# Kernel tuning notes

Hardware: AMD Instinct MI355X
Metric: run time of the kernel (lower is better)

Reference implementation:

```python
import jax, jax.numpy as jnp
import numpy as np

B, N, D, H, F = 2, 2048, 512, 8, 8
HD = D // H

def setup_inputs() -> dict:
    key = jax.random.key(0)
    ks = jax.random.split(key, 11)
    s = 1.0 / np.sqrt(D)
    return {
        "x": jax.random.normal(ks[0], (B, N, D), dtype=jnp.float32),
        "phase_coords": jax.random.uniform(ks[1], (B, N, F), dtype=jnp.float32) * 6.28,
        "Wq": jax.random.normal(ks[2], (D, D), dtype=jnp.float32) * s,
        "bq": jax.random.normal(ks[3], (D,), dtype=jnp.float32) * 0.01,
        "Wk": jax.random.normal(ks[4], (D, D), dtype=jnp.float32) * s,
        "bk": jax.random.normal(ks[5], (D,), dtype=jnp.float32) * 0.01,
        "Wv": jax.random.normal(ks[6], (D, D), dtype=jnp.float32) * s,
        "bv": jax.random.normal(ks[7], (D,), dtype=jnp.float32) * 0.01,
        "Wo": jax.random.normal(ks[8], (D, D), dtype=jnp.float32) * s,
        "bo": jax.random.normal(ks[9], (D,), dtype=jnp.float32) * 0.01,
        "phase_bias": jax.random.normal(ks[10], (H, F), dtype=jnp.float32) * 0.1,
    }

def reference(x, phase_coords, Wq, bq, Wk, bk, Wv, bv, Wo, bo, phase_bias):
    b, n, _ = x.shape
    def proj(W, bias):
        # [B,N,D] -> [B,H,N,HD]
        return (x @ W.T + bias).reshape(b, n, H, HD).transpose(0, 2, 1, 3)
    Q, K, V = proj(Wq, bq), proj(Wk, bk), proj(Wv, bv)
    scores = jnp.einsum("bhqd,bhkd->bhqk", Q, K) / np.sqrt(HD)
    # phase coherence bias: cos of pairwise phase diffs, weighted per head
    phase_diff = phase_coords[:, :, None, :] - phase_coords[:, None, :, :]  # [B,N,N,F]
    coherence = jnp.cos(phase_diff)
    bias = jnp.einsum("bqkf,hf->bhqk", coherence, phase_bias)
    scores = scores + bias
    attn = jax.nn.softmax(scores, axis=-1)
    attended = jnp.einsum("bhqk,bhkd->bhqd", attn, V)
    attended = attended.transpose(0, 2, 1, 3).reshape(b, n, D)
    return attended @ Wo.T + bo
```

## Files before the change

### kernel.cpp

```cpp
#include <hip/hip_runtime.h>
#include <stdint.h>

typedef unsigned short u16;
typedef unsigned int   u32;
typedef __bf16 bf16x8 __attribute__((ext_vector_type(8)));
typedef float  f32x4  __attribute__((ext_vector_type(4)));
typedef u16    u16x8  __attribute__((ext_vector_type(8)));
typedef u16    u16x4  __attribute__((ext_vector_type(4)));

#define B_  2
#define N_  2048
#define D_  512
#define H_  8
#define HD_ 64
#define LOG2E 1.4426950408889634f

__device__ __forceinline__ u16 f2bf(float f) {
  union { float f; u32 u; } v; v.f = f;
  u32 r = v.u + 0x7FFFu + ((v.u >> 16) & 1u);
  return (u16)(r >> 16);
}
__device__ __forceinline__ u16 f2bf_trunc(float f) {
  union { float f; u32 u; } v; v.f = f;
  return (u16)(v.u >> 16);
}
__device__ __forceinline__ float bf2f(u16 s) {
  union { u32 u; float f; } v; v.u = ((u32)s) << 16; return v.f;
}
__device__ __forceinline__ void gload_lds16(const void* g, void* l) {
  __builtin_amdgcn_global_load_lds(
      (const __attribute__((address_space(1))) void*)g,
      (__attribute__((address_space(3))) void*)l, 16, 0, 0);
}
__device__ __forceinline__ void gload_lds4(const void* g, void* l) {
  __builtin_amdgcn_global_load_lds(
      (const __attribute__((address_space(1))) void*)g,
      (__attribute__((address_space(3))) void*)l, 4, 0, 0);
}

__global__ __launch_bounds__(256) void k_prep(
    const float* __restrict__ x, const float* __restrict__ pc,
    const float* __restrict__ Wq, const float* __restrict__ bq,
    const float* __restrict__ Wk, const float* __restrict__ bk,
    const float* __restrict__ Wv, const float* __restrict__ bv,
    const float* __restrict__ Wo,
    u16* __restrict__ xb, u16* __restrict__ wqkvb, float* __restrict__ bqkv,
    u16* __restrict__ wob, u16* __restrict__ pcs)
{
  int gid = blockIdx.x * blockDim.x + threadIdx.x;
  int stride = gridDim.x * blockDim.x;
  const float qs = 0.125f * LOG2E;
  for (int i = gid; i < B_ * N_ * D_; i += stride) xb[i] = f2bf(x[i]);
  for (int i = gid; i < 3 * D_ * D_; i += stride) {
    int r = i >> 9;
    float v;
    if (r < 512)       v = Wq[i] * qs;
    else if (r < 1024) v = Wk[i - 512 * 512];
    else               v = Wv[i - 1024 * 512];
    wqkvb[i] = f2bf(v);
  }
  for (int i = gid; i < 3 * D_; i += stride) {
    float v;
    if (i < 512)       v = bq[i] * qs;
    else if (i < 1024) v = bk[i - 512];
    else               v = bv[i - 1024];
    bqkv[i] = v;
  }
  for (int i = gid; i < D_ * D_; i += stride) wob[i] = f2bf(Wo[i]);
  for (int i = gid; i < B_ * N_; i += stride) {
#pragma unroll
    for (int f = 0; f < 8; f++) {
      float a = pc[i * 8 + f];
      pcs[i * 16 + f]     = f2bf(__cosf(a));
      pcs[i * 16 + 8 + f] = f2bf(__sinf(a));
    }
  }
}

template <int MODE, int BN>
__global__ __launch_bounds__(256) void k_gemm(
    const u16* __restrict__ A, const u16* __restrict__ Bm,
    const float* __restrict__ bias,
    u16* __restrict__ Qp, u16* __restrict__ Kp, u16* __restrict__ Vt,
    float* __restrict__ Of)
{
  constexpr int JT  = BN / 32;
  constexpr int BNC = BN / 32;
  __shared__ u16 As[3][64 * 64];
  __shared__ u16 Bs[3][BN * 64];
  const int tid = threadIdx.x;
  const int wave = tid >> 6, lane = tid & 63;
  const int fr = lane & 15, kg = lane >> 4;
  const int m0 = blockIdx.x * 64, n0 = blockIdx.y * BN;
  const int wr = (wave >> 1) * 32, wc = (wave & 1) * (BN / 2);

  f32x4 acc[2][JT];
#pragma unroll
  for (int i = 0; i < 2; i++)
#pragma unroll
    for (int j = 0; j < JT; j++)
#pragma unroll
      for (int r = 0; r < 4; r++) acc[i][j][r] = 0.f;

  auto stage = [&](int buf, int k0) {
#pragma unroll
    for (int u = 0; u < 2; u++) {
      int chunk = (wave * 2 + u) * 64 + lane;
      int row = chunk >> 3, cl = chunk & 7;
      gload_lds16(A + (size_t)(m0 + row) * 512 + k0 + ((cl ^ (row & 7)) << 3),
                  &As[buf][(wave * 2 + u) * 512]);
    }
#pragma unroll
    for (int u = 0; u < BNC; u++) {
      int chunk = (wave * BNC + u) * 64 + lane;
      int row = chunk >> 3, cl = chunk & 7;
      gload_lds16(Bm + (size_t)(n0 + row) * 512 + k0 + ((cl ^ (row & 7)) << 3),
                  &Bs[buf][(wave * BNC + u) * 512]);
    }
  };

  stage(0, 0);
  stage(1, 64);

#pragma unroll
  for (int s = 0; s < 8; s++) {
    if (s < 7) {
      if constexpr (BN == 128) asm volatile("s_waitcnt vmcnt(6)" ::: "memory");
      else                     asm volatile("s_waitcnt vmcnt(4)" ::: "memory");
    } else {
      asm volatile("s_waitcnt vmcnt(0)" ::: "memory");
    }
    asm volatile("s_waitcnt lgkmcnt(0)" ::: "memory");
    __builtin_amdgcn_sched_barrier(0);
    __builtin_amdgcn_s_barrier();
    __builtin_amdgcn_sched_barrier(0);
    if (s < 6) stage((s + 2) % 3, (s + 2) * 64);
    const int cb = s % 3;
#pragma unroll
    for (int ksub = 0; ksub < 2; ksub++) {
      bf16x8 af[2], bf[JT];
#pragma unroll
      for (int i = 0; i < 2; i++)
        af[i] = *(const bf16x8*)&As[cb][(wr + i * 16 + fr) * 64 + (((ksub * 4 + kg) ^ (fr & 7)) << 3)];
#pragma unroll
      for (int j = 0; j < JT; j++)
        bf[j] = *(const bf16x8*)&Bs[cb][(wc + j * 16 + fr) * 64 + (((ksub * 4 + kg) ^ (fr & 7)) << 3)];
#pragma unroll
      for (int i = 0; i < 2; i++)
#pragma unroll
        for (int j = 0; j < JT; j++)
          acc[i][j] = __builtin_amdgcn_mfma_f32_16x16x32_bf16(af[i], bf[j], acc[i][j], 0, 0, 0);
    }
  }

  if (MODE == 1) {
#pragma unroll
    for (int j = 0; j < JT; j++) {
      int col = n0 + wc + j * 16 + fr;
      float bc = bias[col];
#pragma unroll
      for (int i = 0; i < 2; i++)
#pragma unroll
        for (int r = 0; r < 4; r++)
          Of[(size_t)(m0 + wr + i * 16 + kg * 4 + r) * 512 + col] = acc[i][j][r] + bc;
  } } else {
    const int seg = n0 >> 9;
    const int nb = n0 & 511;
    if (seg < 2) {
      u16* dst = seg ? Kp : Qp;
#pragma unroll
      for (int j = 0; j < JT; j++) {
        int col = nb + wc + j * 16 + fr;
        float bc = bias[n0 + wc + j * 16 + fr];
#pragma unroll
        for (int i = 0; i < 2; i++)
#pragma unroll
          for (int r = 0; r < 4; r++)
            dst[(size_t)(m0 + wr + i * 16 + kg * 4 + r) * 512 + col] = f2bf(acc[i][j][r] + bc);
      }
    } else {
#pragma unroll
      for (int j = 0; j < JT; j++) {
        int cc = nb + wc + j * 16 + fr;
        float bc = bias[n0 + wc + j * 16 + fr];
        int h = cc >> 6, d = cc & 63;
#pragma unroll
        for (int i = 0; i < 2; i++) {
          int row = m0 + wr + i * 16 + kg * 4;
          int b = row >> 11, n = row & 2047;
          u16x4 o;
#pragma unroll
          for (int r = 0; r < 4; r++) o[r] = f2bf(acc[i][j][r] + bc);
          *(u16x4*)&Vt[((size_t)(b * 8 + h) * 64 + d) * N_ + n] = o;
        }
      }
    }
  }
}

__global__ __launch_bounds__(256, 4) void k_attn(
    const u16* __restrict__ Qp, const u16* __restrict__ Kp,
    const u16* __restrict__ Vt, const u16* __restrict__ pcs,
    const float* __restrict__ pb, u16* __restrict__ attb,
    float* __restrict__ attO, float* __restrict__ attL, int split)
{
  const int bh = blockIdx.y, b = bh >> 3, h = bh & 7;
  const int q0 = blockIdx.x * 128;
  const int z = blockIdx.z;
  const int ntile = 32 / split;
  const int kvbase = z * ntile * 64;
  const int tid = threadIdx.x, wave = tid >> 6, lane = tid & 63;
  const int fr = lane & 15, kg = lane >> 4;

  __shared__ u16 Klds[2][64 * 64];
  __shared__ u16 Vlds[2][64 * 64];
  __shared__ u16 Ke[2][64 * 16];
  __shared__ u16 Plds[4][32 * 64];

  auto stageKV = [&](int buf, int kv) {
#pragma unroll
    for (int p = 0; p < 2; p++) {
      int c = p * 256 + tid;
      int row = c >> 3, c8 = c & 7;
      gload_lds16(Kp + (size_t)(b * N_ + kv + row) * 512 + h * 64 + ((c8 ^ (row & 7)) << 3),
                  &Klds[buf][p * 2048 + wave * 512]);
      gload_lds16(Vt + (size_t)(bh * 64 + row) * N_ + kv + ((c8 ^ (row & 7)) << 3),
                  &Vlds[buf][p * 2048 + wave * 512]);
      int er = c >> 3, ec = (c & 7) * 2;
      gload_lds4(pcs + (size_t)(b * N_ + kv + er) * 16 + ec,
                 &Ke[buf][p * 512 + wave * 128]);
    }
  };

  bf16x8 qa[2][3];
#pragma unroll
  for (int i = 0; i < 2; i++) {
    int gq = b * N_ + q0 + wave * 32 + i * 16 + fr;
#pragma unroll
    for (int ks = 0; ks < 2; ks++)
      qa[i][ks] = *(const bf16x8*)&Qp[(size_t)gq * D_ + h * HD_ + ks * 32 + kg * 8];
    union { bf16x8 v; u16 s[8]; } qe;
    if (kg < 2) {
      u16x8 cs = *(const u16x8*)&pcs[(size_t)gq * 16 + kg * 8];
#pragma unroll
      for (int j = 0; j < 8; j++) qe.s[j] = f2bf(pb[h * 8 + j] * LOG2E * bf2f(cs[j]));
    } else {
#pragma unroll
      for (int j = 0; j < 8; j++) qe.s[j] = 0;
    }
    qa[i][2] = qe.v;
  }

  f32x4 accO[2][4];
#pragma unroll
  for (int i = 0; i < 2; i++)
#pragma unroll
    for (int d = 0; d < 4; d++)
#pragma unroll
      for (int r = 0; r < 4; r++) accO[i][d][r] = 0.f;
  float Lacc[2][4];
#pragma unroll
  for (int i = 0; i < 2; i++)
#pragma unroll
    for (int r = 0; r < 4; r++) Lacc[i][r] = 0.f;

  union { u16x8 u; bf16x8 b; } zf;
#pragma unroll
  for (int t = 0; t < 8; t++) zf.u[t] = 0;

  stageKV(0, kvbase);
  stageKV(1, kvbase + 64);

  for (int t = 0; t < ntile; t++) {
    const int cb = t & 1;
    if (t < ntile - 1) asm volatile("s_waitcnt vmcnt(6)" ::: "memory");
    else               asm volatile("s_waitcnt vmcnt(0)" ::: "memory");
    __builtin_amdgcn_sched_barrier(0);
    __builtin_amdgcn_s_barrier();
    __builtin_amdgcn_sched_barrier(0);

    f32x4 accS[2][4];
#pragma unroll
    for (int i = 0; i < 2; i++)
#pragma unroll
      for (int j = 0; j < 4; j++)
#pragma unroll
        for (int r = 0; r < 4; r++) accS[i][j][r] = 0.f;

    __builtin_amdgcn_s_setprio(1);
#pragma unroll
    for (int ks = 0; ks < 2; ks++) {
#pragma unroll
      for (int j = 0; j < 4; j++) {
        bf16x8 kb = *(const bf16x8*)&Klds[cb][(j * 16 + fr) * 64 + (((ks * 4 + kg) ^ (fr & 7)) << 3)];
#pragma unroll
        for (int i = 0; i < 2; i++)
          accS[i][j] = __builtin_amdgcn_mfma_f32_16x16x32_bf16(qa[i][ks], kb, accS[i][j], 0, 0, 0);
      }
    }
#pragma unroll
    for (int j = 0; j < 4; j++) {
      bf16x8 kbe = zf.b;
      if (kg < 2) kbe = *(const bf16x8*)&Ke[cb][(j * 16 + fr) * 16 + kg * 8];
#pragma unroll
      for (int i = 0; i < 2; i++)
        accS[i][j] = __builtin_amdgcn_mfma_f32_16x16x32_bf16(qa[i][2], kbe, accS[i][j], 0, 0, 0);
    }
    __builtin_amdgcn_s_setprio(0);

#pragma unroll
    for (int i = 0; i < 2; i++) {
#pragma unroll
      for (int j = 0; j < 4; j++) {
#pragma unroll
        for (int r = 0; r < 4; r++) {
          float p = __builtin_amdgcn_exp2f(accS[i][j][r] - 11.5415603f);
          Lacc[i][r] += p;
          int rw = i * 16 + kg * 4 + r;
          Plds[wave][rw * 64 + ((j * 16 + fr) ^ ((rw & 7) << 3))] = f2bf_trunc(p);
        }
      }
    }
    asm volatile("s_waitcnt lgkmcnt(0)" ::: "memory");
    __builtin_amdgcn_sched_barrier(0);

    __builtin_amdgcn_s_setprio(1);
#pragma unroll
    for (int ks = 0; ks < 2; ks++) {
      bf16x8 pa[2];
#pragma unroll
      for (int i = 0; i < 2; i++)
        pa[i] = *(const bf16x8*)&Plds[wave][(i * 16 + fr) * 64 + ((ks * 32 + kg * 8) ^ ((fr & 7) << 3))];
#pragma unroll
      for (int d = 0; d < 4; d++) {
        bf16x8 vb = *(const bf16x8*)&Vlds[cb][(d * 16 + fr) * 64 + (((ks * 4 + kg) ^ (fr & 7)) << 3)];
#pragma unroll
        for (int i = 0; i < 2; i++)
          accO[i][d] = __builtin_amdgcn_mfma_f32_16x16x32_bf16(pa[i], vb, accO[i][d], 0, 0, 0);
      }
    }
    __builtin_amdgcn_s_setprio(0);

    asm volatile("s_waitcnt lgkmcnt(0)" ::: "memory");
    __builtin_amdgcn_sched_barrier(0);
    __builtin_amdgcn_s_barrier();
    __builtin_amdgcn_sched_barrier(0);
    if (t + 2 < ntile) stageKV(cb, kvbase + (t + 2) * 64);
  }

#pragma unroll
  for (int i = 0; i < 2; i++) {
#pragma unroll
    for (int r = 0; r < 4; r++) {
      float l = Lacc[i][r];
      l += __shfl_xor(l, 1); l += __shfl_xor(l, 2);
      l += __shfl_xor(l, 4); l += __shfl_xor(l, 8);
      int qg = q0 + wave * 32 + i * 16 + kg * 4 + r;
      if (split == 1) {
        float inv = 1.0f / l;
#pragma unroll
        for (int d = 0; d < 4; d++)
          attb[(size_t)(b * N_ + qg) * 512 + h * 64 + d * 16 + fr] = f2bf(accO[i][d][r] * inv);
      } else {
        if (fr == 0) attL[((size_t)z * 16 + bh) * N_ + qg] = l;
#pragma unroll
        for (int d = 0; d < 4; d++)
          attO[(((size_t)z * 16 + bh) * N_ + qg) * 64 + d * 16 + fr] = accO[i][d][r];
      }
    }
  }
}

__global__ __launch_bounds__(256) void k_merge(
    const float* __restrict__ attO, const float* __restrict__ attL,
    u16* __restrict__ attb, int split)
{
  int idx = blockIdx.x * 256 + threadIdx.x;
  int stride = gridDim.x * 256;
  for (; idx < 16 * N_ * 16; idx += stride) {
    int bh = idx >> 15, rem = idx & 32767;
    int q = rem >> 4, d4 = rem & 15;
    size_t obase = ((size_t)bh * N_ + q) * 64 + d4 * 4;
    f32x4 o = *(const f32x4*)&attO[obase];
    float L = attL[(size_t)bh * N_ + q];
    for (int s = 1; s < split; s++) {
      o += *(const f32x4*)&attO[(size_t)s * 16 * N_ * 64 + obase];
      L += attL[(size_t)s * 16 * N_ + (size_t)bh * N_ + q];
    }
    float inv = 1.0f / L;
    u16x4 w;
#pragma unroll
    for (int r = 0; r < 4; r++) w[r] = f2bf(o[r] * inv);
    *(u16x4*)&attb[((size_t)(bh >> 3) * N_ + q) * 512 + (bh & 7) * 64 + d4 * 4] = w;
  }
}

extern "C" void kernel_launch(void* const* d_in, const int* in_sizes, int n_in,
                              void* d_out, int out_size, void* d_ws, size_t ws_size,
                              hipStream_t stream)
{
  (void)in_sizes; (void)n_in; (void)out_size;
  const float* x  = (const float*)d_in[0];
  const float* pc = (const float*)d_in[1];
  const float* Wq = (const float*)d_in[2];
  const float* bq = (const float*)d_in[3];
  const float* Wk = (const float*)d_in[4];
  const float* bk = (const float*)d_in[5];
  const float* Wv = (const float*)d_in[6];
  const float* bv = (const float*)d_in[7];
  const float* Wo = (const float*)d_in[8];
  const float* bo = (const float*)d_in[9];
  const float* pb = (const float*)d_in[10];

  u16* ws = (u16*)d_ws;
  const size_t TOK = (size_t)B_ * N_;
  u16* xb    = ws;
  u16* Qp    = xb    + TOK * D_;
  u16* Kp    = Qp    + TOK * D_;
  u16* Vt    = Kp    + TOK * D_;
  u16* attb  = Vt    + TOK * D_;
  u16* wqkvb = attb  + TOK * D_;
  u16* wob   = wqkvb + (size_t)3 * D_ * D_;
  u16* pcs   = wob   + (size_t)D_ * D_;
  float* bqkv = (float*)(pcs + TOK * 16);
  const size_t fixed_u16 = (size_t)(pcs - ws) + TOK * 16 + 3072;

  const size_t per_split_u16 = (size_t)16 * N_ * 2 + (size_t)16 * N_ * 64 * 2;
  int S = 1;
  if (ws_size >= (fixed_u16 + 4 * per_split_u16) * 2) S = 4;
  else if (ws_size >= (fixed_u16 + 2 * per_split_u16) * 2) S = 2;
  float* attL = (float*)(ws + fixed_u16);
  float* attO = attL + (size_t)S * 16 * N_;

  k_prep<<<1024, 256, 0, stream>>>(x, pc, Wq, bq, Wk, bk, Wv, bv, Wo,
                                   xb, wqkvb, bqkv, wob, pcs);
  k_gemm<0, 128><<<dim3(64, 12), 256, 0, stream>>>(xb, wqkvb, bqkv, Qp, Kp, Vt, nullptr);
  k_attn<<<dim3(16, 16, S), 256, 0, stream>>>(Qp, Kp, Vt, pcs, pb, attb, attO, attL, S);
  if (S > 1) k_merge<<<1024, 256, 0, stream>>>(attO, attL, attb, S);
  k_gemm<1, 64><<<dim3(64, 8), 256, 0, stream>>>(attb, wob, bo, nullptr, nullptr, nullptr, (float*)d_out);
}
```

Baseline: 151.8 us.

## Pack phase features into head-major Q/K rows, drop split-KV and merge kernel

Q and K are now written head-major with 96-element rows: 64 projection dims plus 32 slots holding the precomputed per-head weighted cos/sin phase terms, with zero padding. The attention kernel loads K as one 96-wide tile, runs the phase bias as a third MFMA k-step, and single-buffers V with a staggered prefetch. Split-KV, its merge kernel, and the per-tile Ke staging are removed, and occupancy hints drop from 4 to 3 blocks. This trades fewer launches and simpler staging for more workspace traffic and a grid of only 256 blocks with no KV split.

```diff
diff --git a/kernel.cpp b/kernel.cpp
--- a/kernel.cpp
+++ b/kernel.cpp
@@ -13,6 +13,7 @@
 #define D_  512
 #define H_  8
 #define HD_ 64
+#define QKD 96
 #define LOG2E 1.4426950408889634f
 
 __device__ __forceinline__ u16 f2bf(float f) {
@@ -24,18 +25,10 @@
   union { float f; u32 u; } v; v.f = f;
   return (u16)(v.u >> 16);
 }
-__device__ __forceinline__ float bf2f(u16 s) {
-  union { u32 u; float f; } v; v.u = ((u32)s) << 16; return v.f;
-}
 __device__ __forceinline__ void gload_lds16(const void* g, void* l) {
   __builtin_amdgcn_global_load_lds(
       (const __attribute__((address_space(1))) void*)g,
       (__attribute__((address_space(3))) void*)l, 16, 0, 0);
-}
-__device__ __forceinline__ void gload_lds4(const void* g, void* l) {
-  __builtin_amdgcn_global_load_lds(
-      (const __attribute__((address_space(1))) void*)g,
-      (__attribute__((address_space(3))) void*)l, 4, 0, 0);
 }
 
 __global__ __launch_bounds__(256) void k_prep(
@@ -43,9 +36,9 @@
     const float* __restrict__ Wq, const float* __restrict__ bq,
     const float* __restrict__ Wk, const float* __restrict__ bk,
     const float* __restrict__ Wv, const float* __restrict__ bv,
-    const float* __restrict__ Wo,
+    const float* __restrict__ Wo, const float* __restrict__ pb,
     u16* __restrict__ xb, u16* __restrict__ wqkvb, float* __restrict__ bqkv,
-    u16* __restrict__ wob, u16* __restrict__ pcs)
+    u16* __restrict__ wob, u16* __restrict__ Qe, u16* __restrict__ Ke)
 {
   int gid = blockIdx.x * blockDim.x + threadIdx.x;
   int stride = gridDim.x * blockDim.x;
@@ -67,13 +60,25 @@
     bqkv[i] = v;
   }
   for (int i = gid; i < D_ * D_; i += stride) wob[i] = f2bf(Wo[i]);
-  for (int i = gid; i < B_ * N_; i += stride) {
+
+  for (int i = gid; i < 16 * N_; i += stride) {
+    int bh = i >> 11, n = i & 2047;
+    int b = bh >> 3, h = bh & 7;
+    u16x8 qc, qsn, kc, ksn, z;
 #pragma unroll
     for (int f = 0; f < 8; f++) {
-      float a = pc[i * 8 + f];
-      pcs[i * 16 + f]     = f2bf(__cosf(a));
-      pcs[i * 16 + 8 + f] = f2bf(__sinf(a));
-    }
+      float a = pc[((size_t)b * N_ + n) * 8 + f];
+      float cv = __cosf(a), sv = __sinf(a);
+      float w = pb[h * 8 + f] * LOG2E;
+      qc[f]  = f2bf(w * cv);  qsn[f] = f2bf(w * sv);
+      kc[f]  = f2bf(cv);      ksn[f] = f2bf(sv);
+      z[f] = 0;
+    }
+    size_t base = ((size_t)bh * N_ + n) * QKD;
+    *(u16x8*)&Qe[base + 64] = qc;  *(u16x8*)&Qe[base + 72] = qsn;
+    *(u16x8*)&Qe[base + 80] = z;   *(u16x8*)&Qe[base + 88] = z;
+    *(u16x8*)&Ke[base + 64] = kc;  *(u16x8*)&Ke[base + 72] = ksn;
+    *(u16x8*)&Ke[base + 80] = z;   *(u16x8*)&Ke[base + 88] = z;
   }
 }
 
@@ -81,7 +86,7 @@
 __global__ __launch_bounds__(256) void k_gemm(
     const u16* __restrict__ A, const u16* __restrict__ Bm,
     const float* __restrict__ bias,
-    u16* __restrict__ Qp, u16* __restrict__ Kp, u16* __restrict__ Vt,
+    u16* __restrict__ Qe, u16* __restrict__ Ke, u16* __restrict__ Vt,
     float* __restrict__ Of)
 {
   constexpr int JT  = BN / 32;
@@ -167,16 +172,21 @@
     const int seg = n0 >> 9;
     const int nb = n0 & 511;
     if (seg < 2) {
-      u16* dst = seg ? Kp : Qp;
+      u16* dst = seg ? Ke : Qe;
 #pragma unroll
       for (int j = 0; j < JT; j++) {
         int col = nb + wc + j * 16 + fr;
         float bc = bias[n0 + wc + j * 16 + fr];
-#pragma unroll
-        for (int i = 0; i < 2; i++)
-#pragma unroll
-          for (int r = 0; r < 4; r++)
-            dst[(size_t)(m0 + wr + i * 16 + kg * 4 + r) * 512 + col] = f2bf(acc[i][j][r] + bc);
+        int h = col >> 6, d = col & 63;
+#pragma unroll
+        for (int i = 0; i < 2; i++) {
+#pragma unroll
+          for (int r = 0; r < 4; r++) {
+            int row = m0 + wr + i * 16 + kg * 4 + r;
+            int b = row >> 11, nn = row & 2047;
+            dst[((size_t)(b * 8 + h) * N_ + nn) * QKD + d] = f2bf(acc[i][j][r] + bc);
+          }
+        }
       }
     } else {
 #pragma unroll
@@ -198,57 +208,46 @@
   }
 }
 
-__global__ __launch_bounds__(256, 4) void k_attn(
-    const u16* __restrict__ Qp, const u16* __restrict__ Kp,
-    const u16* __restrict__ Vt, const u16* __restrict__ pcs,
-    const float* __restrict__ pb, u16* __restrict__ attb,
-    float* __restrict__ attO, float* __restrict__ attL, int split)
+__global__ __launch_bounds__(256, 3) void k_attn(
+    const u16* __restrict__ Qe, const u16* __restrict__ Ke,
+    const u16* __restrict__ Vt, u16* __restrict__ attb)
 {
-  const int bh = blockIdx.y, b = bh >> 3, h = bh & 7;
-  const int q0 = blockIdx.x * 128;
-  const int z = blockIdx.z;
-  const int ntile = 32 / split;
-  const int kvbase = z * ntile * 64;
+  const int bh = blockIdx.x, b = bh >> 3, h = bh & 7;
+  const int q0 = blockIdx.y * 128;
   const int tid = threadIdx.x, wave = tid >> 6, lane = tid & 63;
   const int fr = lane & 15, kg = lane >> 4;
 
-  __shared__ u16 Klds[2][64 * 64];
-  __shared__ u16 Vlds[2][64 * 64];
-  __shared__ u16 Ke[2][64 * 16];
+  __shared__ u16 Klds[2][64 * 96];
+  __shared__ u16 Vlds[64 * 64];
   __shared__ u16 Plds[4][32 * 64];
 
-  auto stageKV = [&](int buf, int kv) {
+  auto stageK = [&](int buf, int kv) {
+#pragma unroll
+    for (int p = 0; p < 3; p++) {
+      u32 c = p * 256 + tid;
+      u32 r = c / 12u, s = c - r * 12u;
+      u32 g = (s < 8) ? (s ^ (r & 7)) : (8 + ((s & 3) ^ (r & 3)));
+      gload_lds16(Ke + ((size_t)bh * N_ + kv + r) * QKD + g * 8,
+                  &Klds[buf][(p * 256 + wave * 64) * 8]);
+    }
+  };
+  auto stageV = [&](int kv) {
 #pragma unroll
     for (int p = 0; p < 2; p++) {
       int c = p * 256 + tid;
       int row = c >> 3, c8 = c & 7;
-      gload_lds16(Kp + (size_t)(b * N_ + kv + row) * 512 + h * 64 + ((c8 ^ (row & 7)) << 3),
-                  &Klds[buf][p * 2048 + wave * 512]);
-      gload_lds16(Vt + (size_t)(bh * 64 + row) * N_ + kv + ((c8 ^ (row & 7)) << 3),
-                  &Vlds[buf][p * 2048 + wave * 512]);
-      int er = c >> 3, ec = (c & 7) * 2;
-      gload_lds4(pcs + (size_t)(b * N_ + kv + er) * 16 + ec,
-                 &Ke[buf][p * 512 + wave * 128]);
+      gload_lds16(Vt + ((size_t)bh * 64 + row) * N_ + kv + ((c8 ^ (row & 7)) << 3),
+                  &Vlds[(p * 256 + wave * 64) * 8]);
     }
   };
 
   bf16x8 qa[2][3];
 #pragma unroll
   for (int i = 0; i < 2; i++) {
-    int gq = b * N_ + q0 + wave * 32 + i * 16 + fr;
-#pragma unroll
-    for (int ks = 0; ks < 2; ks++)
-      qa[i][ks] = *(const bf16x8*)&Qp[(size_t)gq * D_ + h * HD_ + ks * 32 + kg * 8];
-    union { bf16x8 v; u16 s[8]; } qe;
-    if (kg < 2) {
-      u16x8 cs = *(const u16x8*)&pcs[(size_t)gq * 16 + kg * 8];
-#pragma unroll
-      for (int j = 0; j < 8; j++) qe.s[j] = f2bf(pb[h * 8 + j] * LOG2E * bf2f(cs[j]));
-    } else {
-#pragma unroll
-      for (int j = 0; j < 8; j++) qe.s[j] = 0;
-    }
-    qa[i][2] = qe.v;
+    size_t gq = (size_t)bh * N_ + q0 + wave * 32 + i * 16 + fr;
+#pragma unroll
+    for (int ks = 0; ks < 3; ks++)
+      qa[i][ks] = *(const bf16x8*)&Qe[gq * QKD + ks * 32 + kg * 8];
   }
 
   f32x4 accO[2][4];
@@ -264,17 +263,14 @@
 #pragma unroll
     for (int r = 0; r < 4; r++) Lacc[i][r] = 0.f;
 
-  union { u16x8 u; bf16x8 b; } zf;
-#pragma unroll
-  for (int t = 0; t < 8; t++) zf.u[t] = 0;
-
-  stageKV(0, kvbase);
-  stageKV(1, kvbase + 64);
-
-  for (int t = 0; t < ntile; t++) {
+  stageK(0, 0);
+  stageV(0);
+  stageK(1, 64);
+
+  for (int t = 0; t < 32; t++) {
     const int cb = t & 1;
-    if (t < ntile - 1) asm volatile("s_waitcnt vmcnt(6)" ::: "memory");
-    else               asm volatile("s_waitcnt vmcnt(0)" ::: "memory");
+    if (t < 31) asm volatile("s_waitcnt vmcnt(3)" ::: "memory");
+    else        asm volatile("s_waitcnt vmcnt(0)" ::: "memory");
     __builtin_amdgcn_sched_barrier(0);
     __builtin_amdgcn_s_barrier();
     __builtin_amdgcn_sched_barrier(0);
@@ -289,22 +285,15 @@
 
     __builtin_amdgcn_s_setprio(1);
 #pragma unroll
-    for (int ks = 0; ks < 2; ks++) {
+    for (int ks = 0; ks < 3; ks++) {
 #pragma unroll
       for (int j = 0; j < 4; j++) {
-        bf16x8 kb = *(const bf16x8*)&Klds[cb][(j * 16 + fr) * 64 + (((ks * 4 + kg) ^ (fr & 7)) << 3)];
+        int slot = (ks < 2) ? ((ks * 4 + kg) ^ (fr & 7)) : (8 + (kg ^ (fr & 3)));
+        bf16x8 kb = *(const bf16x8*)&Klds[cb][(j * 16 + fr) * 96 + slot * 8];
 #pragma unroll
         for (int i = 0; i < 2; i++)
           accS[i][j] = __builtin_amdgcn_mfma_f32_16x16x32_bf16(qa[i][ks], kb, accS[i][j], 0, 0, 0);
       }
-    }
-#pragma unroll
-    for (int j = 0; j < 4; j++) {
-      bf16x8 kbe = zf.b;
-      if (kg < 2) kbe = *(const bf16x8*)&Ke[cb][(j * 16 + fr) * 16 + kg * 8];
-#pragma unroll
-      for (int i = 0; i < 2; i++)
-        accS[i][j] = __builtin_amdgcn_mfma_f32_16x16x32_bf16(qa[i][2], kbe, accS[i][j], 0, 0, 0);
     }
     __builtin_amdgcn_s_setprio(0);
 
@@ -333,7 +322,7 @@
         pa[i] = *(const bf16x8*)&Plds[wave][(i * 16 + fr) * 64 + ((ks * 32 + kg * 8) ^ ((fr & 7) << 3))];
 #pragma unroll
       for (int d = 0; d < 4; d++) {
-        bf16x8 vb = *(const bf16x8*)&Vlds[cb][(d * 16 + fr) * 64 + (((ks * 4 + kg) ^ (fr & 7)) << 3)];
+        bf16x8 vb = *(const bf16x8*)&Vlds[(d * 16 + fr) * 64 + (((ks * 4 + kg) ^ (fr & 7)) << 3)];
 #pragma unroll
         for (int i = 0; i < 2; i++)
           accO[i][d] = __builtin_amdgcn_mfma_f32_16x16x32_bf16(pa[i], vb, accO[i][d], 0, 0, 0);
@@ -341,11 +330,11 @@
     }
     __builtin_amdgcn_s_setprio(0);
 
-    asm volatile("s_waitcnt lgkmcnt(0)" ::: "memory");
     __builtin_amdgcn_sched_barrier(0);
     __builtin_amdgcn_s_barrier();
     __builtin_amdgcn_sched_barrier(0);
-    if (t + 2 < ntile) stageKV(cb, kvbase + (t + 2) * 64);
+    if (t + 1 < 32) stageV((t + 1) * 64);
+    if (t + 2 < 32) stageK(cb, (t + 2) * 64);
   }
 
 #pragma unroll
@@ -355,43 +344,12 @@
       float l = Lacc[i][r];
       l += __shfl_xor(l, 1); l += __shfl_xor(l, 2);
       l += __shfl_xor(l, 4); l += __shfl_xor(l, 8);
+      float inv = 1.0f / l;
       int qg = q0 + wave * 32 + i * 16 + kg * 4 + r;
-      if (split == 1) {
-        float inv = 1.0f / l;
-#pragma unroll
-        for (int d = 0; d < 4; d++)
-          attb[(size_t)(b * N_ + qg) * 512 + h * 64 + d * 16 + fr] = f2bf(accO[i][d][r] * inv);
-      } else {
-        if (fr == 0) attL[((size_t)z * 16 + bh) * N_ + qg] = l;
-#pragma unroll
-        for (int d = 0; d < 4; d++)
-          attO[(((size_t)z * 16 + bh) * N_ + qg) * 64 + d * 16 + fr] = accO[i][d][r];
-      }
-    }
-  }
-}
-
-__global__ __launch_bounds__(256) void k_merge(
-    const float* __restrict__ attO, const float* __restrict__ attL,
-    u16* __restrict__ attb, int split)
-{
-  int idx = blockIdx.x * 256 + threadIdx.x;
-  int stride = gridDim.x * 256;
-  for (; idx < 16 * N_ * 16; idx += stride) {
-    int bh = idx >> 15, rem = idx & 32767;
-    int q = rem >> 4, d4 = rem & 15;
-    size_t obase = ((size_t)bh * N_ + q) * 64 + d4 * 4;
-    f32x4 o = *(const f32x4*)&attO[obase];
-    float L = attL[(size_t)bh * N_ + q];
-    for (int s = 1; s < split; s++) {
-      o += *(const f32x4*)&attO[(size_t)s * 16 * N_ * 64 + obase];
-      L += attL[(size_t)s * 16 * N_ + (size_t)bh * N_ + q];
-    }
-    float inv = 1.0f / L;
-    u16x4 w;
-#pragma unroll
-    for (int r = 0; r < 4; r++) w[r] = f2bf(o[r] * inv);
-    *(u16x4*)&attb[((size_t)(bh >> 3) * N_ + q) * 512 + (bh & 7) * 64 + d4 * 4] = w;
+#pragma unroll
+      for (int d = 0; d < 4; d++)
+        attb[(size_t)(b * N_ + qg) * 512 + h * 64 + d * 16 + fr] = f2bf(accO[i][d][r] * inv);
+    }
   }
 }
 
@@ -399,7 +357,7 @@
                               void* d_out, int out_size, void* d_ws, size_t ws_size,
                               hipStream_t stream)
 {
-  (void)in_sizes; (void)n_in; (void)out_size;
+  (void)in_sizes; (void)n_in; (void)out_size; (void)ws_size;
   const float* x  = (const float*)d_in[0];
   const float* pc = (const float*)d_in[1];
   const float* Wq = (const float*)d_in[2];
@@ -415,27 +373,17 @@
   u16* ws = (u16*)d_ws;
   const size_t TOK = (size_t)B_ * N_;
   u16* xb    = ws;
-  u16* Qp    = xb    + TOK * D_;
-  u16* Kp    = Qp    + TOK * D_;
-  u16* Vt    = Kp    + TOK * D_;
+  u16* Qe    = xb    + TOK * D_;
+  u16* Ke    = Qe    + (size_t)16 * N_ * QKD;
+  u16* Vt    = Ke    + (size_t)16 * N_ * QKD;
   u16* attb  = Vt    + TOK * D_;
   u16* wqkvb = attb  + TOK * D_;
   u16* wob   = wqkvb + (size_t)3 * D_ * D_;
-  u16* pcs   = wob   + (size_t)D_ * D_;
-  float* bqkv = (float*)(pcs + TOK * 16);
-  const size_t fixed_u16 = (size_t)(pcs - ws) + TOK * 16 + 3072;
-
-  const size_t per_split_u16 = (size_t)16 * N_ * 2 + (size_t)16 * N_ * 64 * 2;
-  int S = 1;
-  if (ws_size >= (fixed_u16 + 4 * per_split_u16) * 2) S = 4;
-  else if (ws_size >= (fixed_u16 + 2 * per_split_u16) * 2) S = 2;
-  float* attL = (float*)(ws + fixed_u16);
-  float* attO = attL + (size_t)S * 16 * N_;
-
-  k_prep<<<1024, 256, 0, stream>>>(x, pc, Wq, bq, Wk, bk, Wv, bv, Wo,
-                                   xb, wqkvb, bqkv, wob, pcs);
-  k_gemm<0, 128><<<dim3(64, 12), 256, 0, stream>>>(xb, wqkvb, bqkv, Qp, Kp, Vt, nullptr);
-  k_attn<<<dim3(16, 16, S), 256, 0, stream>>>(Qp, Kp, Vt, pcs, pb, attb, attO, attL, S);
-  if (S > 1) k_merge<<<1024, 256, 0, stream>>>(attO, attL, attb, S);
+  float* bqkv = (float*)(wob + (size_t)D_ * D_);
+
+  k_prep<<<1024, 256, 0, stream>>>(x, pc, Wq, bq, Wk, bk, Wv, bv, Wo, pb,
+                                   xb, wqkvb, bqkv, wob, Qe, Ke);
+  k_gemm<0, 128><<<dim3(64, 12), 256, 0, stream>>>(xb, wqkvb, bqkv, Qe, Ke, Vt, nullptr);
+  k_attn<<<dim3(16, 16), 256, 0, stream>>>(Qe, Ke, Vt, attb);
   k_gemm<1, 64><<<dim3(64, 8), 256, 0, stream>>>(attb, wob, bo, nullptr, nullptr, nullptr, (float*)d_out);
 }
```

After: 158.4 us. 1.04x slower.
